# Kernel tuning notes

Measured on AMD Instinct MI355X. Metric: run time of the kernel, lower is better.

Reference implementation:

```python
import jax, jax.numpy as jnp
import numpy as np

VX, VY = 0.2, 0.2
X_OFF = VX / 2 + 0.0      # pc_range x_min = 0
Y_OFF = VY / 2 + (-40.0)  # pc_range y_min = -40
BN_EPS = 1e-3


def setup_inputs() -> dict:
    key = jax.random.key(0)
    k1, k2, k3, k4, k5, k6 = jax.random.split(key, 6)
    K, P, C_IN, C_AUG, C_OUT = 20000, 100, 4, 9, 64
    features = jax.random.normal(k1, (K, P, C_IN), dtype=jnp.float32)
    # at least 1 point per pillar (avoids div-by-zero, as in real voxelization)
    num_voxels = jax.random.randint(k2, (K,), 1, P + 1, dtype=jnp.int64)
    coors = jax.random.randint(k3, (K, 4), 0, 352, dtype=jnp.int64)
    W = jax.random.normal(k4, (C_AUG, C_OUT), dtype=jnp.float32) * (1.0 / np.sqrt(C_AUG))
    gamma = jnp.ones((C_OUT,), dtype=jnp.float32) + 0.1 * jax.random.normal(k5, (C_OUT,), dtype=jnp.float32)
    beta = 0.1 * jax.random.normal(k6, (C_OUT,), dtype=jnp.float32)
    return {"features": features, "num_voxels": num_voxels, "coors": coors,
            "W": W, "gamma": gamma, "beta": beta}


def reference(features, num_voxels, coors, W, gamma, beta):
    K, P, _ = features.shape
    dt = features.dtype
    pn = num_voxels.astype(dt)[:, None, None]                      # [K,1,1]
    cx = coors[:, 3].astype(dt)[:, None] * VX + X_OFF              # [K,1]
    cy = coors[:, 2].astype(dt)[:, None] * VY + Y_OFF              # [K,1]
    mask = (jnp.arange(P)[None, :] < num_voxels[:, None]).astype(dt)[..., None]  # [K,P,1]
    # cluster offset: point xyz minus per-pillar mean
    points_mean = features[..., :3].sum(axis=-2, keepdims=True) / pn
    f_cluster = features[..., :3] - points_mean                    # [K,P,3]
    # center offset: point xy minus pillar center
    f_center = jnp.stack([features[..., 0] - cx, features[..., 1] - cy], axis=-1)  # [K,P,2]
    feats = jnp.concatenate([features, f_cluster, f_center], axis=-1) * mask       # [K,P,9]
    # PFNLayer: Linear(no bias) -> BatchNorm1d (training-mode batch stats) -> ReLU -> max over points
    x = jnp.einsum('kpc,cu->kpu', feats, W)                        # [K,P,64]
    mu = x.mean(axis=(0, 1))
    var = ((x - mu) ** 2).mean(axis=(0, 1))
    x = (x - mu) * jax.lax.rsqrt(var + BN_EPS) * gamma + beta
    x = jax.nn.relu(x)
    return x.max(axis=1)                                           # [K,64] (squeezed)
```

## Files before the change

kernel.cpp:

```cpp
#include <hip/hip_runtime.h>


#define NBLK 1280

__device__ __forceinline__ float wred63(float v) {
  int t;
  t = __builtin_amdgcn_update_dpp(0, __float_as_int(v), 0xB1, 0xf, 0xf, true);
  v += __int_as_float(t);
  t = __builtin_amdgcn_update_dpp(0, __float_as_int(v), 0x4E, 0xf, 0xf, true);
  v += __int_as_float(t);
  t = __builtin_amdgcn_update_dpp(0, __float_as_int(v), 0x141, 0xf, 0xf, true);
  v += __int_as_float(t);
  t = __builtin_amdgcn_update_dpp(0, __float_as_int(v), 0x140, 0xf, 0xf, true);
  v += __int_as_float(t);
  t = __builtin_amdgcn_update_dpp(0, __float_as_int(v), 0x142, 0xa, 0xf, true);
  v += __int_as_float(t);
  t = __builtin_amdgcn_update_dpp(0, __float_as_int(v), 0x143, 0xc, 0xf, true);
  v += __int_as_float(t);
  return v;
}
__device__ __forceinline__ float wsum_bcast(float v) {
  return __int_as_float(
      __builtin_amdgcn_readlane(__float_as_int(wred63(v)), 63));
}

__global__ void __launch_bounds__(256) pfn_main(
    const float4* __restrict__ feat, const int* __restrict__ nvox,
    const int* __restrict__ coors, int K, int P, int cnt,
    const float* __restrict__ W, const float* __restrict__ gamma,
    float* __restrict__ p54, float4* __restrict__ ext,
    float4* __restrict__ rec) {
  __shared__ float4 pts[4][108];
  __shared__ float red[4][56];
  const int lane = threadIdx.x & 63;
  const int wid = threadIdx.x >> 6;
  const int q = lane & 15;
  const int g = lane >> 4;

  int sa = 0, sb = 0, ub = 0, ub2 = 0;
  if (lane >= 14 && lane < 34) { sa = (lane - 14) / 5; sb = (lane - 14) % 5; }
  if (lane >= 39 && lane < 54) {
    int r2 = lane - 39, b = 0;
    while (r2 >= 5 - b) { r2 -= 5 - b; ++b; }
    ub = b; ub2 = b + r2;
  }

  const float4* Wq = (const float4*)W;
  const float4 g4 = ((const float4*)gamma)[q];
  float4 sg;
  sg.x = (g4.x >= 0.f) ? 1.f : -1.f;
  sg.y = (g4.y >= 0.f) ? 1.f : -1.f;
  sg.z = (g4.z >= 0.f) ? 1.f : -1.f;
  sg.w = (g4.w >= 0.f) ? 1.f : -1.f;
  float4 wx, wy, wz, w3;
  {
    float4 t0 = Wq[0 * 16 + q], t1 = Wq[4 * 16 + q], t2 = Wq[7 * 16 + q];
    wx.x = (t0.x + t1.x + t2.x) * sg.x; wx.y = (t0.y + t1.y + t2.y) * sg.y;
    wx.z = (t0.z + t1.z + t2.z) * sg.z; wx.w = (t0.w + t1.w + t2.w) * sg.w;
  }
  {
    float4 t0 = Wq[1 * 16 + q], t1 = Wq[5 * 16 + q], t2 = Wq[8 * 16 + q];
    wy.x = (t0.x + t1.x + t2.x) * sg.x; wy.y = (t0.y + t1.y + t2.y) * sg.y;
    wy.z = (t0.z + t1.z + t2.z) * sg.z; wy.w = (t0.w + t1.w + t2.w) * sg.w;
  }
  {
    float4 t0 = Wq[2 * 16 + q], t1 = Wq[6 * 16 + q];
    wz.x = (t0.x + t1.x) * sg.x; wz.y = (t0.y + t1.y) * sg.y;
    wz.z = (t0.z + t1.z) * sg.z; wz.w = (t0.w + t1.w) * sg.w;
  }
  {
    float4 t0 = Wq[3 * 16 + q];
    w3.x = t0.x * sg.x; w3.y = t0.y * sg.y;
    w3.z = t0.z * sg.z; w3.w = t0.w * sg.w;
  }

  float q2[10] = {0, 0, 0, 0, 0, 0, 0, 0, 0, 0};
  float oacc = 0.f;

  const int gw = blockIdx.x * 4 + wid;
  const int k0 = gw * cnt;
  const int kend = (k0 + cnt < K) ? k0 + cnt : K;
  const bool hih = lane < (P - 64);

  for (int k = k0; k < kend; ++k) {
    const size_t base = (size_t)k * P;
    const float4 f0 = feat[base + lane];
    float4 f1;
    if (hih) f1 = feat[base + 64 + lane];
    const int nv = nvox[k];

    pts[wid][lane] = f0;
    if (hih) pts[wid][64 + lane] = f1;

    float sax = f0.x, say = f0.y, saz = f0.z;
    float svx = 0, svy = 0, svz = 0, svw = 0;
    if (lane < nv) {
      svx = f0.x; svy = f0.y; svz = f0.z; svw = f0.w;
      q2[0] = fmaf(f0.x, f0.x, q2[0]); q2[1] = fmaf(f0.x, f0.y, q2[1]);
      q2[2] = fmaf(f0.x, f0.z, q2[2]); q2[3] = fmaf(f0.x, f0.w, q2[3]);
      q2[4] = fmaf(f0.y, f0.y, q2[4]); q2[5] = fmaf(f0.y, f0.z, q2[5]);
      q2[6] = fmaf(f0.y, f0.w, q2[6]); q2[7] = fmaf(f0.z, f0.z, q2[7]);
      q2[8] = fmaf(f0.z, f0.w, q2[8]); q2[9] = fmaf(f0.w, f0.w, q2[9]);
    }
    if (hih) {
      sax += f1.x; say += f1.y; saz += f1.z;
      if (64 + lane < nv) {
        svx += f1.x; svy += f1.y; svz += f1.z; svw += f1.w;
        q2[0] = fmaf(f1.x, f1.x, q2[0]); q2[1] = fmaf(f1.x, f1.y, q2[1]);
        q2[2] = fmaf(f1.x, f1.z, q2[2]); q2[3] = fmaf(f1.x, f1.w, q2[3]);
        q2[4] = fmaf(f1.y, f1.y, q2[4]); q2[5] = fmaf(f1.y, f1.z, q2[5]);
        q2[6] = fmaf(f1.y, f1.w, q2[6]); q2[7] = fmaf(f1.z, f1.z, q2[7]);
        q2[8] = fmaf(f1.z, f1.w, q2[8]); q2[9] = fmaf(f1.w, f1.w, q2[9]);
      }
    }

    const float rx = wsum_bcast(sax);
    const float ry = wsum_bcast(say);
    const float rz = wsum_bcast(saz);
    const float vx = wsum_bcast(svx);
    const float vy = wsum_bcast(svy);
    const float vz = wsum_bcast(svz);
    const float vw = wsum_bcast(svw);

    const float nvf = (float)nv, inv = 1.f / nvf;
    const float cx = (float)coors[k * 4 + 3] * 0.2f + 0.1f;
    const float cy = (float)coors[k * 4 + 2] * 0.2f - 39.9f;
    const float o0 = -rx * inv, o1 = -ry * inv, o2 = -rz * inv;
    const float o3 = -cx, o4 = -cy;

    {
      float add = 0.f;
      if (lane < 4) {
        add = (lane == 0) ? vx : (lane == 1) ? vy : (lane == 2) ? vz : vw;
      } else if (lane >= 14 && lane < 34) {
        const float sva = (sa == 0) ? vx : (sa == 1) ? vy : (sa == 2) ? vz : vw;
        const float ob = (sb == 0) ? o0 : (sb == 1) ? o1
                       : (sb == 2) ? o2 : (sb == 3) ? o3 : o4;
        add = sva * ob;
      } else if (lane >= 34 && lane < 39) {
        const int b = lane - 34;
        const float ob = (b == 0) ? o0 : (b == 1) ? o1
                       : (b == 2) ? o2 : (b == 3) ? o3 : o4;
        add = nvf * ob;
      } else if (lane >= 39 && lane < 54) {
        const float oa = (ub == 0) ? o0 : (ub == 1) ? o1
                       : (ub == 2) ? o2 : (ub == 3) ? o3 : o4;
        const float ob = (ub2 == 0) ? o0 : (ub2 == 1) ? o1
                       : (ub2 == 2) ? o2 : (ub2 == 3) ? o3 : o4;
        add = nvf * oa * ob;
      }
      oacc += add;
    }

    if (lane == 0) {
      float4 r0; r0.x = vx; r0.y = vy; r0.z = vz; r0.w = vw;
      float4 r1; r1.x = rx; r1.y = ry; r1.z = rz; r1.w = nvf;
      rec[2 * (size_t)k] = r0;
      rec[2 * (size_t)k + 1] = r1;
    }

    float4 m4 = {-3e38f, -3e38f, -3e38f, -3e38f};
    int p = 0;
    for (; p + 8 <= nv; p += 8) {
      const float4 fa = pts[wid][p + g];
      const float4 fb = pts[wid][p + 4 + g];
      m4.x = fmaxf(m4.x, fmaf(fa.x, wx.x, fmaf(fa.y, wy.x, fmaf(fa.z, wz.x, fa.w * w3.x))));
      m4.y = fmaxf(m4.y, fmaf(fa.x, wx.y, fmaf(fa.y, wy.y, fmaf(fa.z, wz.y, fa.w * w3.y))));
      m4.z = fmaxf(m4.z, fmaf(fa.x, wx.z, fmaf(fa.y, wy.z, fmaf(fa.z, wz.z, fa.w * w3.z))));
      m4.w = fmaxf(m4.w, fmaf(fa.x, wx.w, fmaf(fa.y, wy.w, fmaf(fa.z, wz.w, fa.w * w3.w))));
      m4.x = fmaxf(m4.x, fmaf(fb.x, wx.x, fmaf(fb.y, wy.x, fmaf(fb.z, wz.x, fb.w * w3.x))));
      m4.y = fmaxf(m4.y, fmaf(fb.x, wx.y, fmaf(fb.y, wy.y, fmaf(fb.z, wz.y, fb.w * w3.y))));
      m4.z = fmaxf(m4.z, fmaf(fb.x, wx.z, fmaf(fb.y, wy.z, fmaf(fb.z, wz.z, fb.w * w3.z))));
      m4.w = fmaxf(m4.w, fmaf(fb.x, wx.w, fmaf(fb.y, wy.w, fmaf(fb.z, wz.w, fb.w * w3.w))));
    }
    if (p < nv) {
      const int i0 = p + g, i1 = p + 4 + g;
      const float4 fa = pts[wid][i0];
      const float4 fb = pts[wid][i1];
      if (i0 < nv) {
        m4.x = fmaxf(m4.x, fmaf(fa.x, wx.x, fmaf(fa.y, wy.x, fmaf(fa.z, wz.x, fa.w * w3.x))));
        m4.y = fmaxf(m4.y, fmaf(fa.x, wx.y, fmaf(fa.y, wy.y, fmaf(fa.z, wz.y, fa.w * w3.y))));
        m4.z = fmaxf(m4.z, fmaf(fa.x, wx.z, fmaf(fa.y, wy.z, fmaf(fa.z, wz.z, fa.w * w3.z))));
        m4.w = fmaxf(m4.w, fmaf(fa.x, wx.w, fmaf(fa.y, wy.w, fmaf(fa.z, wz.w, fa.w * w3.w))));
      }
      if (i1 < nv) {
        m4.x = fmaxf(m4.x, fmaf(fb.x, wx.x, fmaf(fb.y, wy.x, fmaf(fb.z, wz.x, fb.w * w3.x))));
        m4.y = fmaxf(m4.y, fmaf(fb.x, wx.y, fmaf(fb.y, wy.y, fmaf(fb.z, wz.y, fb.w * w3.y))));
        m4.z = fmaxf(m4.z, fmaf(fb.x, wx.z, fmaf(fb.y, wy.z, fmaf(fb.z, wz.z, fb.w * w3.z))));
        m4.w = fmaxf(m4.w, fmaf(fb.x, wx.w, fmaf(fb.y, wy.w, fmaf(fb.z, wz.w, fb.w * w3.w))));
      }
    }
    m4.x = fmaxf(m4.x, __shfl_xor(m4.x, 16, 64));
    m4.y = fmaxf(m4.y, __shfl_xor(m4.y, 16, 64));
    m4.z = fmaxf(m4.z, __shfl_xor(m4.z, 16, 64));
    m4.w = fmaxf(m4.w, __shfl_xor(m4.w, 16, 64));
    m4.x = fmaxf(m4.x, __shfl_xor(m4.x, 32, 64));
    m4.y = fmaxf(m4.y, __shfl_xor(m4.y, 32, 64));
    m4.z = fmaxf(m4.z, __shfl_xor(m4.z, 32, 64));
    m4.w = fmaxf(m4.w, __shfl_xor(m4.w, 32, 64));
    if (lane < 16) ext[(size_t)k * 16 + q] = m4;
  }

  if (lane < 54 && (lane < 4 || lane >= 14)) red[wid][lane] = oacc;
#pragma unroll
  for (int i = 0; i < 10; ++i) q2[i] = wred63(q2[i]);
  if (lane == 63) {
#pragma unroll
    for (int i = 0; i < 10; ++i) red[wid][4 + i] = q2[i];
  }
  __syncthreads();
  const int t = threadIdx.x;
  if (t < 54) {
    p54[t * NBLK + blockIdx.x] =
        red[0][t] + red[1][t] + red[2][t] + red[3][t];
  }
}

__global__ void __launch_bounds__(256) pfn_finalize(
    const float* __restrict__ p54, const float* __restrict__ W,
    const float* __restrict__ gamma, const float* __restrict__ beta,
    float invN, float* __restrict__ ss) {
  __shared__ float msum[54];
  __shared__ float m54[54];
  const int t = threadIdx.x;
  const int r = t >> 2, j = t & 3;
  if (r < 54) {
    const int chunk = NBLK >> 2;
    const float* row = p54 + (size_t)r * NBLK + j * chunk;
    float a0 = 0, a1 = 0, a2 = 0, a3 = 0, a4 = 0, a5 = 0, a6 = 0, a7 = 0;
    int b = 0;
    for (; b + 8 <= chunk; b += 8) {
      a0 += row[b];     a1 += row[b + 1]; a2 += row[b + 2]; a3 += row[b + 3];
      a4 += row[b + 4]; a5 += row[b + 5]; a6 += row[b + 6]; a7 += row[b + 7];
    }
    for (; b < chunk; ++b) a0 += row[b];
    float s = ((a0 + a1) + (a2 + a3)) + ((a4 + a5) + (a6 + a7));
    s += __shfl_xor(s, 1, 64);
    s += __shfl_xor(s, 2, 64);
    if (j == 0) msum[r] = s;
  }
  __syncthreads();
  if (t < 54) {
    float v;
    if (t < 9) {
      const int g2 = (t < 4) ? t : (t < 7 ? t - 4 : t - 7);
      v = msum[g2];
      if (t >= 4) v += msum[34 + (t - 4)];
    } else {
      int r2 = t - 9, c = 0;
      while (r2 >= 9 - c) { r2 -= 9 - c; ++c; }
      const int c2 = c + r2;
      const int a = (c < 4) ? c : (c < 7 ? c - 4 : c - 7);
      const int b2 = (c2 < 4) ? c2 : (c2 < 7 ? c2 - 4 : c2 - 7);
      const int lo = a < b2 ? a : b2, hi = a < b2 ? b2 : a;
      v = msum[4 + lo * (9 - lo) / 2 + (hi - lo)];
      if (c2 >= 4) v += msum[14 + a * 5 + (c2 - 4)];
      if (c >= 4) v += msum[14 + b2 * 5 + (c - 4)];
      if (c >= 4 && c2 >= 4) {
        const int ua = c - 4, ub = c2 - 4;
        v += msum[39 + ua * 5 - ua * (ua - 1) / 2 + (ub - ua)];
      }
    }
    m54[t] = v;
  }
  __syncthreads();
  if (t < 64) {
    float wc[9];
#pragma unroll
    for (int c = 0; c < 9; ++c) wc[c] = W[c * 64 + t];
    float mu = 0.f;
#pragma unroll
    for (int c = 0; c < 9; ++c) mu += m54[c] * invN * wc[c];
    float ex2 = 0.f;
    int idx = 9;
#pragma unroll
    for (int c = 0; c < 9; ++c)
#pragma unroll
      for (int c2 = c; c2 < 9; ++c2) {
        float v = m54[idx] * invN * wc[c] * wc[c2];
        ex2 += (c == c2) ? v : 2.f * v;
        ++idx;
      }
    const float var = ex2 - mu * mu;
    const float scale = gamma[t] * rsqrtf(var + 1e-3f);
    ss[t] = scale;
    ss[64 + t] = beta[t] - mu * scale;
  }
}

__global__ void __launch_bounds__(256) pfn_apply(
    const float4* __restrict__ ext, const float4* __restrict__ rec,
    const int* __restrict__ coors, const float* __restrict__ W,
    const float* __restrict__ ss, int K, int P, float4* __restrict__ out) {
  const int t = blockIdx.x * 256 + threadIdx.x;
  if (t >= K * 16) return;
  const int k = t >> 4, j = t & 15;

  const float4* Wq = (const float4*)W;
  const float4 v4 = Wq[4 * 16 + j], v5 = Wq[5 * 16 + j];
  const float4 v6 = Wq[6 * 16 + j], v7 = Wq[7 * 16 + j];
  const float4 v8 = Wq[8 * 16 + j];

  const float4 e = ext[t];
  const float4 rb = rec[2 * (size_t)k + 1];
  const float nvf = rb.w, inv = 1.f / nvf;
  const float cx = (float)coors[k * 4 + 3] * 0.2f + 0.1f;
  const float cy = (float)coors[k * 4 + 2] * 0.2f - 39.9f;
  const float o0 = -rb.x * inv, o1 = -rb.y * inv, o2 = -rb.z * inv;
  float4 bias;
  bias.x = v4.x * o0 + v5.x * o1 + v6.x * o2 - v7.x * cx - v8.x * cy;
  bias.y = v4.y * o0 + v5.y * o1 + v6.y * o2 - v7.y * cx - v8.y * cy;
  bias.z = v4.z * o0 + v5.z * o1 + v6.z * o2 - v7.z * cx - v8.z * cy;
  bias.w = v4.w * o0 + v5.w * o1 + v6.w * o2 - v7.w * cx - v8.w * cy;

  const float4 sc = ((const float4*)ss)[j];
  const float4 sh = ((const float4*)(ss + 64))[j];
  const bool masked = nvf < (float)P;

  float4 o;
  {
    const float sgn = (sc.x >= 0.f) ? 1.f : -1.f;
    float ev = sgn * e.x + bias.x;
    if (masked) ev = (sc.x >= 0.f) ? fmaxf(ev, 0.f) : fminf(ev, 0.f);
    o.x = fmaxf(fmaf(sc.x, ev, sh.x), 0.f);
  }
  {
    const float sgn = (sc.y >= 0.f) ? 1.f : -1.f;
    float ev = sgn * e.y + bias.y;
    if (masked) ev = (sc.y >= 0.f) ? fmaxf(ev, 0.f) : fminf(ev, 0.f);
    o.y = fmaxf(fmaf(sc.y, ev, sh.y), 0.f);
  }
  {
    const float sgn = (sc.z >= 0.f) ? 1.f : -1.f;
    float ev = sgn * e.z + bias.z;
    if (masked) ev = (sc.z >= 0.f) ? fmaxf(ev, 0.f) : fminf(ev, 0.f);
    o.z = fmaxf(fmaf(sc.z, ev, sh.z), 0.f);
  }
  {
    const float sgn = (sc.w >= 0.f) ? 1.f : -1.f;
    float ev = sgn * e.w + bias.w;
    if (masked) ev = (sc.w >= 0.f) ? fmaxf(ev, 0.f) : fminf(ev, 0.f);
    o.w = fmaxf(fmaf(sc.w, ev, sh.w), 0.f);
  }
  out[t] = o;
}

extern "C" void kernel_launch(void* const* d_in, const int* in_sizes, int n_in,
                              void* d_out, int out_size, void* d_ws,
                              size_t ws_size, hipStream_t stream) {
  const float4* feat = (const float4*)d_in[0];
  const int* nvox = (const int*)d_in[1];
  const int* coors = (const int*)d_in[2];
  const float* W = (const float*)d_in[3];
  const float* gamma = (const float*)d_in[4];
  const float* beta = (const float*)d_in[5];

  const int K = in_sizes[1];
  const int P = in_sizes[0] / (K * 4);

  float* ss = (float*)d_ws;
  float4* ext = (float4*)(ss + 128);
  float4* rec = ext + (size_t)K * 16;
  float* p54 = (float*)(rec + (size_t)K * 2);

  const int nwaves = NBLK * 4;
  const int cnt = (K + nwaves - 1) / nwaves;

  pfn_main<<<NBLK, 256, 0, stream>>>(feat, nvox, coors, K, P, cnt, W, gamma,
                                     p54, ext, rec);
  pfn_finalize<<<1, 256, 0, stream>>>(p54, W, gamma, beta,
                                      1.0f / (float)((long long)K * P), ss);
  pfn_apply<<<(K * 16 + 255) / 256, 256, 0, stream>>>(ext, rec, coors, W, ss,
                                                      K, P, (float4*)d_out);
}
```

Baseline: 42.80 us.

## Use packed f32x2 math in pillar max loop and raise block count

Rewrites the per-point linear/max inner loop and the second-moment accumulation with 2-wide float vectors, so the compiler can emit packed FMA/max instructions (v_pk_fma_f32). Raises the main kernel's block count from 1280 to 2048, adds an occupancy hint of 6 in launch_bounds, and widens the finalize kernel to 512 threads to reduce the larger partial array. The aim is to cut VALU instruction count and spread the pillars over more waves. The cost is more partial sums to reduce and possible register pressure under the tighter occupancy bound.

```diff
diff --git a/kernel.cpp b/kernel.cpp
--- a/kernel.cpp
+++ b/kernel.cpp
@@ -1,7 +1,9 @@
 #include <hip/hip_runtime.h>
 
 
-#define NBLK 1280
+typedef float f32x2 __attribute__((ext_vector_type(2)));
+
+#define NBLK 2048
 
 __device__ __forceinline__ float wred63(float v) {
   int t;
@@ -24,7 +26,7 @@
       __builtin_amdgcn_readlane(__float_as_int(wred63(v)), 63));
 }
 
-__global__ void __launch_bounds__(256) pfn_main(
+__global__ void __launch_bounds__(256, 6) pfn_main(
     const float4* __restrict__ feat, const int* __restrict__ nvox,
     const int* __restrict__ coors, int K, int P, int cnt,
     const float* __restrict__ W, const float* __restrict__ gamma,
@@ -45,36 +47,24 @@
     ub = b; ub2 = b + r2;
   }
 
-  const float4* Wq = (const float4*)W;
-  const float4 g4 = ((const float4*)gamma)[q];
-  float4 sg;
-  sg.x = (g4.x >= 0.f) ? 1.f : -1.f;
-  sg.y = (g4.y >= 0.f) ? 1.f : -1.f;
-  sg.z = (g4.z >= 0.f) ? 1.f : -1.f;
-  sg.w = (g4.w >= 0.f) ? 1.f : -1.f;
-  float4 wx, wy, wz, w3;
-  {
-    float4 t0 = Wq[0 * 16 + q], t1 = Wq[4 * 16 + q], t2 = Wq[7 * 16 + q];
-    wx.x = (t0.x + t1.x + t2.x) * sg.x; wx.y = (t0.y + t1.y + t2.y) * sg.y;
-    wx.z = (t0.z + t1.z + t2.z) * sg.z; wx.w = (t0.w + t1.w + t2.w) * sg.w;
-  }
-  {
-    float4 t0 = Wq[1 * 16 + q], t1 = Wq[5 * 16 + q], t2 = Wq[8 * 16 + q];
-    wy.x = (t0.x + t1.x + t2.x) * sg.x; wy.y = (t0.y + t1.y + t2.y) * sg.y;
-    wy.z = (t0.z + t1.z + t2.z) * sg.z; wy.w = (t0.w + t1.w + t2.w) * sg.w;
-  }
-  {
-    float4 t0 = Wq[2 * 16 + q], t1 = Wq[6 * 16 + q];
-    wz.x = (t0.x + t1.x) * sg.x; wz.y = (t0.y + t1.y) * sg.y;
-    wz.z = (t0.z + t1.z) * sg.z; wz.w = (t0.w + t1.w) * sg.w;
-  }
-  {
-    float4 t0 = Wq[3 * 16 + q];
-    w3.x = t0.x * sg.x; w3.y = t0.y * sg.y;
-    w3.z = t0.z * sg.z; w3.w = t0.w * sg.w;
-  }
-
-  float q2[10] = {0, 0, 0, 0, 0, 0, 0, 0, 0, 0};
+  const f32x2* W2 = (const f32x2*)W;
+  const int ja = 2 * q, jb = 2 * q + 1;
+  const f32x2 ga = ((const f32x2*)gamma)[ja];
+  const f32x2 gb = ((const f32x2*)gamma)[jb];
+  f32x2 sga, sgb;
+  sga.x = (ga.x >= 0.f) ? 1.f : -1.f; sga.y = (ga.y >= 0.f) ? 1.f : -1.f;
+  sgb.x = (gb.x >= 0.f) ? 1.f : -1.f; sgb.y = (gb.y >= 0.f) ? 1.f : -1.f;
+  const f32x2 wx01 = (W2[0 * 32 + ja] + W2[4 * 32 + ja] + W2[7 * 32 + ja]) * sga;
+  const f32x2 wx23 = (W2[0 * 32 + jb] + W2[4 * 32 + jb] + W2[7 * 32 + jb]) * sgb;
+  const f32x2 wy01 = (W2[1 * 32 + ja] + W2[5 * 32 + ja] + W2[8 * 32 + ja]) * sga;
+  const f32x2 wy23 = (W2[1 * 32 + jb] + W2[5 * 32 + jb] + W2[8 * 32 + jb]) * sgb;
+  const f32x2 wz01 = (W2[2 * 32 + ja] + W2[6 * 32 + ja]) * sga;
+  const f32x2 wz23 = (W2[2 * 32 + jb] + W2[6 * 32 + jb]) * sgb;
+  const f32x2 w301 = W2[3 * 32 + ja] * sga;
+  const f32x2 w323 = W2[3 * 32 + jb] * sgb;
+
+  f32x2 pA = {0, 0}, pB = {0, 0}, pC = {0, 0}, pD = {0, 0};
+  float e0 = 0.f, e1 = 0.f;
   float oacc = 0.f;
 
   const int gw = blockIdx.x * 4 + wid;
@@ -96,21 +86,19 @@
     float svx = 0, svy = 0, svz = 0, svw = 0;
     if (lane < nv) {
       svx = f0.x; svy = f0.y; svz = f0.z; svw = f0.w;
-      q2[0] = fmaf(f0.x, f0.x, q2[0]); q2[1] = fmaf(f0.x, f0.y, q2[1]);
-      q2[2] = fmaf(f0.x, f0.z, q2[2]); q2[3] = fmaf(f0.x, f0.w, q2[3]);
-      q2[4] = fmaf(f0.y, f0.y, q2[4]); q2[5] = fmaf(f0.y, f0.z, q2[5]);
-      q2[6] = fmaf(f0.y, f0.w, q2[6]); q2[7] = fmaf(f0.z, f0.z, q2[7]);
-      q2[8] = fmaf(f0.z, f0.w, q2[8]); q2[9] = fmaf(f0.w, f0.w, q2[9]);
+      const f32x2 f01 = {f0.x, f0.y}, f23 = {f0.z, f0.w};
+      const f32x2 f32r = {f0.w, f0.z};
+      pA += f01 * f01; pB += f01 * f23; pC += f01 * f32r; pD += f23 * f23;
+      e0 = fmaf(f0.x, f0.y, e0); e1 = fmaf(f0.z, f0.w, e1);
     }
     if (hih) {
       sax += f1.x; say += f1.y; saz += f1.z;
       if (64 + lane < nv) {
         svx += f1.x; svy += f1.y; svz += f1.z; svw += f1.w;
-        q2[0] = fmaf(f1.x, f1.x, q2[0]); q2[1] = fmaf(f1.x, f1.y, q2[1]);
-        q2[2] = fmaf(f1.x, f1.z, q2[2]); q2[3] = fmaf(f1.x, f1.w, q2[3]);
-        q2[4] = fmaf(f1.y, f1.y, q2[4]); q2[5] = fmaf(f1.y, f1.z, q2[5]);
-        q2[6] = fmaf(f1.y, f1.w, q2[6]); q2[7] = fmaf(f1.z, f1.z, q2[7]);
-        q2[8] = fmaf(f1.z, f1.w, q2[8]); q2[9] = fmaf(f1.w, f1.w, q2[9]);
+        const f32x2 f01 = {f1.x, f1.y}, f23 = {f1.z, f1.w};
+        const f32x2 f32r = {f1.w, f1.z};
+        pA += f01 * f01; pB += f01 * f23; pC += f01 * f32r; pD += f23 * f23;
+        e0 = fmaf(f1.x, f1.y, e0); e1 = fmaf(f1.z, f1.w, e1);
       }
     }
 
@@ -159,37 +147,38 @@
       rec[2 * (size_t)k + 1] = r1;
     }
 
-    float4 m4 = {-3e38f, -3e38f, -3e38f, -3e38f};
+    f32x2 m01 = {-3e38f, -3e38f}, m23 = {-3e38f, -3e38f};
     int p = 0;
     for (; p + 8 <= nv; p += 8) {
       const float4 fa = pts[wid][p + g];
       const float4 fb = pts[wid][p + 4 + g];
-      m4.x = fmaxf(m4.x, fmaf(fa.x, wx.x, fmaf(fa.y, wy.x, fmaf(fa.z, wz.x, fa.w * w3.x))));
-      m4.y = fmaxf(m4.y, fmaf(fa.x, wx.y, fmaf(fa.y, wy.y, fmaf(fa.z, wz.y, fa.w * w3.y))));
-      m4.z = fmaxf(m4.z, fmaf(fa.x, wx.z, fmaf(fa.y, wy.z, fmaf(fa.z, wz.z, fa.w * w3.z))));
-      m4.w = fmaxf(m4.w, fmaf(fa.x, wx.w, fmaf(fa.y, wy.w, fmaf(fa.z, wz.w, fa.w * w3.w))));
-      m4.x = fmaxf(m4.x, fmaf(fb.x, wx.x, fmaf(fb.y, wy.x, fmaf(fb.z, wz.x, fb.w * w3.x))));
-      m4.y = fmaxf(m4.y, fmaf(fb.x, wx.y, fmaf(fb.y, wy.y, fmaf(fb.z, wz.y, fb.w * w3.y))));
-      m4.z = fmaxf(m4.z, fmaf(fb.x, wx.z, fmaf(fb.y, wy.z, fmaf(fb.z, wz.z, fb.w * w3.z))));
-      m4.w = fmaxf(m4.w, fmaf(fb.x, wx.w, fmaf(fb.y, wy.w, fmaf(fb.z, wz.w, fb.w * w3.w))));
+      f32x2 ba01 = wx01 * fa.x + wy01 * fa.y + wz01 * fa.z + w301 * fa.w;
+      f32x2 ba23 = wx23 * fa.x + wy23 * fa.y + wz23 * fa.z + w323 * fa.w;
+      f32x2 bb01 = wx01 * fb.x + wy01 * fb.y + wz01 * fb.z + w301 * fb.w;
+      f32x2 bb23 = wx23 * fb.x + wy23 * fb.y + wz23 * fb.z + w323 * fb.w;
+      m01 = __builtin_elementwise_max(m01, ba01);
+      m23 = __builtin_elementwise_max(m23, ba23);
+      m01 = __builtin_elementwise_max(m01, bb01);
+      m23 = __builtin_elementwise_max(m23, bb23);
     }
     if (p < nv) {
       const int i0 = p + g, i1 = p + 4 + g;
       const float4 fa = pts[wid][i0];
       const float4 fb = pts[wid][i1];
       if (i0 < nv) {
-        m4.x = fmaxf(m4.x, fmaf(fa.x, wx.x, fmaf(fa.y, wy.x, fmaf(fa.z, wz.x, fa.w * w3.x))));
-        m4.y = fmaxf(m4.y, fmaf(fa.x, wx.y, fmaf(fa.y, wy.y, fmaf(fa.z, wz.y, fa.w * w3.y))));
-        m4.z = fmaxf(m4.z, fmaf(fa.x, wx.z, fmaf(fa.y, wy.z, fmaf(fa.z, wz.z, fa.w * w3.z))));
-        m4.w = fmaxf(m4.w, fmaf(fa.x, wx.w, fmaf(fa.y, wy.w, fmaf(fa.z, wz.w, fa.w * w3.w))));
+        f32x2 ba01 = wx01 * fa.x + wy01 * fa.y + wz01 * fa.z + w301 * fa.w;
+        f32x2 ba23 = wx23 * fa.x + wy23 * fa.y + wz23 * fa.z + w323 * fa.w;
+        m01 = __builtin_elementwise_max(m01, ba01);
+        m23 = __builtin_elementwise_max(m23, ba23);
       }
       if (i1 < nv) {
-        m4.x = fmaxf(m4.x, fmaf(fb.x, wx.x, fmaf(fb.y, wy.x, fmaf(fb.z, wz.x, fb.w * w3.x))));
-        m4.y = fmaxf(m4.y, fmaf(fb.x, wx.y, fmaf(fb.y, wy.y, fmaf(fb.z, wz.y, fb.w * w3.y))));
-        m4.z = fmaxf(m4.z, fmaf(fb.x, wx.z, fmaf(fb.y, wy.z, fmaf(fb.z, wz.z, fb.w * w3.z))));
-        m4.w = fmaxf(m4.w, fmaf(fb.x, wx.w, fmaf(fb.y, wy.w, fmaf(fb.z, wz.w, fb.w * w3.w))));
-      }
-    }
+        f32x2 bb01 = wx01 * fb.x + wy01 * fb.y + wz01 * fb.z + w301 * fb.w;
+        f32x2 bb23 = wx23 * fb.x + wy23 * fb.y + wz23 * fb.z + w323 * fb.w;
+        m01 = __builtin_elementwise_max(m01, bb01);
+        m23 = __builtin_elementwise_max(m23, bb23);
+      }
+    }
+    float4 m4; m4.x = m01.x; m4.y = m01.y; m4.z = m23.x; m4.w = m23.y;
     m4.x = fmaxf(m4.x, __shfl_xor(m4.x, 16, 64));
     m4.y = fmaxf(m4.y, __shfl_xor(m4.y, 16, 64));
     m4.z = fmaxf(m4.z, __shfl_xor(m4.z, 16, 64));
@@ -201,6 +190,9 @@
     if (lane < 16) ext[(size_t)k * 16 + q] = m4;
   }
 
+  float q2[10];
+  q2[0] = pA.x; q2[1] = e0;   q2[2] = pB.x; q2[3] = pC.x; q2[4] = pA.y;
+  q2[5] = pC.y; q2[6] = pB.y; q2[7] = pD.x; q2[8] = e1;   q2[9] = pD.y;
   if (lane < 54 && (lane < 4 || lane >= 14)) red[wid][lane] = oacc;
 #pragma unroll
   for (int i = 0; i < 10; ++i) q2[i] = wred63(q2[i]);
@@ -216,16 +208,16 @@
   }
 }
 
-__global__ void __launch_bounds__(256) pfn_finalize(
+__global__ void __launch_bounds__(512) pfn_finalize(
     const float* __restrict__ p54, const float* __restrict__ W,
     const float* __restrict__ gamma, const float* __restrict__ beta,
     float invN, float* __restrict__ ss) {
   __shared__ float msum[54];
   __shared__ float m54[54];
   const int t = threadIdx.x;
-  const int r = t >> 2, j = t & 3;
+  const int r = t >> 3, j = t & 7;
   if (r < 54) {
-    const int chunk = NBLK >> 2;
+    const int chunk = NBLK >> 3;
     const float* row = p54 + (size_t)r * NBLK + j * chunk;
     float a0 = 0, a1 = 0, a2 = 0, a3 = 0, a4 = 0, a5 = 0, a6 = 0, a7 = 0;
     int b = 0;
@@ -237,6 +229,7 @@
     float s = ((a0 + a1) + (a2 + a3)) + ((a4 + a5) + (a6 + a7));
     s += __shfl_xor(s, 1, 64);
     s += __shfl_xor(s, 2, 64);
+    s += __shfl_xor(s, 4, 64);
     if (j == 0) msum[r] = s;
   }
   __syncthreads();
@@ -368,7 +361,7 @@
 
   pfn_main<<<NBLK, 256, 0, stream>>>(feat, nvox, coors, K, P, cnt, W, gamma,
                                      p54, ext, rec);
-  pfn_finalize<<<1, 256, 0, stream>>>(p54, W, gamma, beta,
+  pfn_finalize<<<1, 512, 0, stream>>>(p54, W, gamma, beta,
                                       1.0f / (float)((long long)K * P), ss);
   pfn_apply<<<(K * 16 + 255) / 256, 256, 0, stream>>>(ext, rec, coors, W, ss,
                                                       K, P, (float4*)d_out);
```

Result: slower. 52.63 us (+23.0%).
